# Optimization experiments

Hardware: AMD Instinct MI355X
Metric: run time of the kernel (lower is better)

The kernel has to match this reference:

```python
import jax, jax.numpy as jnp
import numpy as np

N_NODES = 50000   # gates in the circuit batch
N_HOPS = 100000   # number of k-hop cones
MAX_PI = 8        # max PIs per hop (padded, masked via stats == -1)
D = 128           # token_emb / hidden
D_FF = 4 * D      # cls_head hidden width (512)
TT = 64           # max_tt_len -> logits width
LN_EPS = 1e-5


def setup_inputs() -> dict:
    key = jax.random.key(0)
    ks = jax.random.split(key, 8)
    hf = jax.random.normal(ks[0], (N_NODES, D), jnp.float32)
    all_hop_pi = jax.random.randint(ks[1], (N_HOPS, MAX_PI), 0, N_NODES)
    # stats in {-1, 0, 1}; -1 marks an invalid (padded) PI slot
    all_hop_pi_stats = jax.random.randint(ks[2], (N_HOPS, MAX_PI), 0, 3) - 1
    all_hop_po = jax.random.randint(ks[3], (N_HOPS,), 0, N_NODES)
    w_q = jax.random.normal(ks[4], (D,), jnp.float32) / np.sqrt(D)
    W1 = jax.random.normal(ks[5], (D, D_FF), jnp.float32) / np.sqrt(D)
    b1 = jnp.zeros((D_FF,), jnp.float32)
    gamma = jnp.ones((D_FF,), jnp.float32)
    beta = jnp.zeros((D_FF,), jnp.float32)
    W2 = jax.random.normal(ks[6], (D_FF, TT), jnp.float32) / np.sqrt(D_FF)
    b2 = jnp.zeros((TT,), jnp.float32)
    return {
        'hf': hf, 'w_q': w_q, 'W1': W1, 'b1': b1, 'gamma': gamma,
        'beta': beta, 'W2': W2, 'b2': b2,
        'all_hop_pi': all_hop_pi, 'all_hop_pi_stats': all_hop_pi_stats,
        'all_hop_po': all_hop_po,
    }


def reference(hf, w_q, W1, b1, gamma, beta, W2, b2,
              all_hop_pi, all_hop_pi_stats, all_hop_po):
    # Per-hop gather: valid PI embeddings + PO embedding -> [H, P+1, D]
    pi_tok = hf[all_hop_pi]                       # [H, P, D]
    po_tok = hf[all_hop_po][:, None, :]           # [H, 1, D]
    tokens = jnp.concatenate([pi_tok, po_tok], axis=1)
    valid = jnp.concatenate(
        [all_hop_pi_stats != -1,
         jnp.ones((all_hop_po.shape[0], 1), bool)], axis=1)  # [H, P+1]
    # tf_Pooling: masked single-query attention pooling over the ragged set
    scores = jnp.einsum('hpd,d->hp', tokens, w_q) / jnp.sqrt(jnp.float32(D))
    scores = jnp.where(valid, scores, jnp.float32(-1e30))
    attn = jax.nn.softmax(scores, axis=-1)
    hop_hf = jnp.einsum('hp,hpd->hd', attn, tokens)  # [H, D]
    # cls_head: Linear(D, 4D) -> ReLU -> LayerNorm(4D) -> Linear(4D, TT)
    h = jax.nn.relu(hop_hf @ W1 + b1)
    mu = jnp.mean(h, axis=-1, keepdims=True)
    var = jnp.var(h, axis=-1, keepdims=True)
    h = (h - mu) * jax.lax.rsqrt(var + LN_EPS) * gamma + beta
    logits = h @ W2 + b2                           # [H, TT]
    return logits
```

## Files before the change

### kernel.cpp

```cpp
#include <hip/hip_runtime.h>
#include <hip/hip_bf16.h>
#include <math.h>

#define DIM 128
#define DFF 512
#define TTW 64
#define NPI 8
#define NTOK 9
#define TILE_H 32

typedef __attribute__((ext_vector_type(8))) short short8;
typedef __attribute__((ext_vector_type(4))) float float4v;

__device__ __forceinline__ float bf16lo_f32(unsigned u) {
    union { unsigned u; float f; } v; v.u = u << 16;
    return v.f;
}
__device__ __forceinline__ float bf16hi_f32(unsigned u) {
    union { unsigned u; float f; } v; v.u = u & 0xffff0000u;
    return v.f;
}
__device__ __forceinline__ unsigned pk_bf16(float a, float b) {
    __hip_bfloat162 h = __float22bfloat162_rn(float2{a, b});
    union { __hip_bfloat162 h; unsigned u; } cv; cv.h = h;
    return cv.u;
}

__global__ __launch_bounds__(256)
void prep_k(const float* __restrict__ hf, const float* __restrict__ W1,
            const float* __restrict__ W2,
            unsigned short* __restrict__ hf2, unsigned short* __restrict__ w1t,
            unsigned short* __restrict__ w2t,
            int n_hf, int B_HF)
{
    __shared__ float tile[32][33];
    const int b = blockIdx.x, t = threadIdx.x;
    if (b < B_HF) {
        int i = (b * 256 + t) * 8;
        if (i < n_hf) {
            float4v v0 = *(const float4v*)(hf + i);
            float4v v1 = *(const float4v*)(hf + i + 4);
            uint4 o;
            o.x = pk_bf16(v0[0], v0[1]);
            o.y = pk_bf16(v0[2], v0[3]);
            o.z = pk_bf16(v1[0], v1[1]);
            o.w = pk_bf16(v1[2], v1[3]);
            *(uint4*)(hf2 + i) = o;
        }
    } else if (b < B_HF + 64) {
        const int tb = b - B_HF;
        const int r0 = (tb & 3) * 32, c0 = (tb >> 2) * 32;
        const int ty = t >> 3, tx = t & 7;
        *(float4v*)&tile[ty][tx * 4] = *(const float4v*)(W1 + (r0 + ty) * DFF + c0 + tx * 4);
        __syncthreads();
        uint2 o;
        o.x = pk_bf16(tile[tx * 4 + 0][ty], tile[tx * 4 + 1][ty]);
        o.y = pk_bf16(tile[tx * 4 + 2][ty], tile[tx * 4 + 3][ty]);
        *(uint2*)(w1t + (c0 + ty) * DIM + r0 + tx * 4) = o;
    } else {
        const int tb = b - B_HF - 64;
        const int r0 = (tb & 15) * 32, c0 = (tb >> 4) * 32;
        const int ty = t >> 3, tx = t & 7;
        *(float4v*)&tile[ty][tx * 4] = *(const float4v*)(W2 + (r0 + ty) * TTW + c0 + tx * 4);
        __syncthreads();
        uint2 o;
        o.x = pk_bf16(tile[tx * 4 + 0][ty], tile[tx * 4 + 1][ty]);
        o.y = pk_bf16(tile[tx * 4 + 2][ty], tile[tx * 4 + 3][ty]);
        *(uint2*)(w2t + (c0 + ty) * DFF + r0 + tx * 4) = o;
    }
}

__global__ __launch_bounds__(256, 3)
void fused_k(const unsigned short* __restrict__ hf2,
             const float* __restrict__ w_q,
             const int* __restrict__ pi,
             const int* __restrict__ stats,
             const int* __restrict__ po,
             const unsigned short* __restrict__ w1t,
             const float* __restrict__ b1,
             const float* __restrict__ gamma,
             const float* __restrict__ beta,
             const unsigned short* __restrict__ w2t,
             const float* __restrict__ b2,
             float* __restrict__ out,
             int H)
{
    __shared__ __align__(16) unsigned short Apool[TILE_H][DIM + 8];
    __shared__ __align__(16) unsigned short Hsm[TILE_H][DFF + 8];
    __shared__ float part[2][16][4][2];

    const int t    = threadIdx.x;
    const int lane = t & 63;
    const int w    = t >> 6;
    const int row  = lane & 15;
    const int quad = lane >> 4;
    const int hop0 = blockIdx.x * TILE_H;

    {
        const int g = t >> 5, l = t & 31;
        const float4v wq4 = *(const float4v*)(w_q + l * 4);

        int idxs[4][NTOK];
        unsigned vm[4];
        #pragma unroll
        for (int it = 0; it < 4; ++it) {
            int hop = hop0 + g + it * 8;
            if (hop >= H) hop = H - 1;
            int4 p0 = *(const int4*)(pi + hop * NPI);
            int4 p1 = *(const int4*)(pi + hop * NPI + 4);
            int4 s0 = *(const int4*)(stats + hop * NPI);
            int4 s1 = *(const int4*)(stats + hop * NPI + 4);
            idxs[it][0] = p0.x; idxs[it][1] = p0.y;
            idxs[it][2] = p0.z; idxs[it][3] = p0.w;
            idxs[it][4] = p1.x; idxs[it][5] = p1.y;
            idxs[it][6] = p1.z; idxs[it][7] = p1.w;
            idxs[it][8] = po[hop];
            vm[it] = (s0.x != -1 ? 1u   : 0u) | (s0.y != -1 ? 2u   : 0u)
                   | (s0.z != -1 ? 4u   : 0u) | (s0.w != -1 ? 8u   : 0u)
                   | (s1.x != -1 ? 16u  : 0u) | (s1.y != -1 ? 32u  : 0u)
                   | (s1.z != -1 ? 64u  : 0u) | (s1.w != -1 ? 128u : 0u)
                   | 256u;
        }
        uint2 tu[4][NTOK];
        #pragma unroll
        for (int it = 0; it < 4; ++it)
            #pragma unroll
            for (int p = 0; p < NTOK; ++p)
                tu[it][p] = *(const uint2*)(hf2 + (size_t)idxs[it][p] * DIM + l * 4);

        #pragma unroll
        for (int it = 0; it < 4; ++it) {
            const int hl = g + it * 8;
            float tok[NTOK][4];
            #pragma unroll
            for (int p = 0; p < NTOK; ++p) {
                tok[p][0] = bf16lo_f32(tu[it][p].x);
                tok[p][1] = bf16hi_f32(tu[it][p].x);
                tok[p][2] = bf16lo_f32(tu[it][p].y);
                tok[p][3] = bf16hi_f32(tu[it][p].y);
            }
            float sc[NTOK];
            #pragma unroll
            for (int p = 0; p < NTOK; ++p)
                sc[p] = tok[p][0]*wq4[0] + tok[p][1]*wq4[1]
                      + tok[p][2]*wq4[2] + tok[p][3]*wq4[3];
            #pragma unroll
            for (int m = 1; m < 32; m <<= 1) {
                #pragma unroll
                for (int p = 0; p < NTOK; ++p) sc[p] += __shfl_xor(sc[p], m);
            }
            const float isd = 0.08838834764831845f;
            float mx = -1e30f;
            #pragma unroll
            for (int p = 0; p < NTOK; ++p) {
                sc[p] = ((vm[it] >> p) & 1u) ? sc[p] * isd : -1e30f;
                mx = fmaxf(mx, sc[p]);
            }
            float se = 0.f;
            #pragma unroll
            for (int p = 0; p < NTOK; ++p) { sc[p] = __expf(sc[p] - mx); se += sc[p]; }
            const float inv = 1.f / se;
            float a0=0.f, a1=0.f, a2=0.f, a3=0.f;
            #pragma unroll
            for (int p = 0; p < NTOK; ++p) {
                float a = sc[p] * inv;
                a0 += a * tok[p][0]; a1 += a * tok[p][1];
                a2 += a * tok[p][2]; a3 += a * tok[p][3];
            }
            uint2 o;
            o.x = pk_bf16(a0, a1);
            o.y = pk_bf16(a2, a3);
            *(uint2*)&Apool[hl][l * 4] = o;
        }
    }
    __syncthreads();

    float4v acc[8][2];
    #pragma unroll
    for (int mt = 0; mt < 8; ++mt) {
        acc[mt][0] = (float4v){0.f, 0.f, 0.f, 0.f};
        acc[mt][1] = (float4v){0.f, 0.f, 0.f, 0.f};
    }
    {
        short8 bfr[2][4];
        #pragma unroll
        for (int ks = 0; ks < 4; ++ks) {
            const int k0 = ks * 32 + quad * 8;
            #pragma unroll
            for (int ht = 0; ht < 2; ++ht)
                bfr[ht][ks] = *(const short8*)&Apool[ht * 16 + row][k0];
        }
        #pragma unroll
        for (int mt = 0; mt < 8; ++mt) {
            const unsigned short* wrow = w1t + (size_t)(w * 128 + mt * 16 + row) * DIM;
            #pragma unroll
            for (int ks = 0; ks < 4; ++ks) {
                short8 afr = *(const short8*)(wrow + ks * 32 + quad * 8);
                acc[mt][0] = __builtin_amdgcn_mfma_f32_16x16x32_bf16(afr, bfr[0][ks], acc[mt][0], 0, 0, 0);
                acc[mt][1] = __builtin_amdgcn_mfma_f32_16x16x32_bf16(afr, bfr[1][ks], acc[mt][1], 0, 0, 0);
            }
        }
    }
    float sum0 = 0.f, ssq0 = 0.f, sum1 = 0.f, ssq1 = 0.f;
    #pragma unroll
    for (int mt = 0; mt < 8; ++mt) {
        const int nb = w * 128 + mt * 16 + quad * 4;
        const float4v bias = *(const float4v*)(b1 + nb);
        #pragma unroll
        for (int r = 0; r < 4; ++r) {
            float v0 = fmaxf(acc[mt][0][r] + bias[r], 0.f);
            float v1 = fmaxf(acc[mt][1][r] + bias[r], 0.f);
            acc[mt][0][r] = v0;  sum0 += v0;  ssq0 += v0 * v0;
            acc[mt][1][r] = v1;  sum1 += v1;  ssq1 += v1 * v1;
        }
    }
    #pragma unroll
    for (int m = 16; m <= 32; m <<= 1) {
        sum0 += __shfl_xor(sum0, m);  ssq0 += __shfl_xor(ssq0, m);
        sum1 += __shfl_xor(sum1, m);  ssq1 += __shfl_xor(ssq1, m);
    }
    if (lane < 16) {
        part[0][row][w][0] = sum0;  part[0][row][w][1] = ssq0;
        part[1][row][w][0] = sum1;  part[1][row][w][1] = ssq1;
    }
    __syncthreads();
    float mu[2], rs[2];
    #pragma unroll
    for (int ht = 0; ht < 2; ++ht) {
        float S = 0.f, Q = 0.f;
        #pragma unroll
        for (int ww = 0; ww < 4; ++ww) {
            S += part[ht][row][ww][0];
            Q += part[ht][row][ww][1];
        }
        const float invn = 1.f / (float)DFF;
        mu[ht] = S * invn;
        float var = Q * invn - mu[ht] * mu[ht];
        rs[ht] = rsqrtf(var + 1e-5f);
    }
    #pragma unroll
    for (int mt = 0; mt < 8; ++mt) {
        const int nb = w * 128 + mt * 16 + quad * 4;
        const float4v g4  = *(const float4v*)(gamma + nb);
        const float4v be4 = *(const float4v*)(beta + nb);
        #pragma unroll
        for (int ht = 0; ht < 2; ++ht) {
            float o[4];
            #pragma unroll
            for (int r = 0; r < 4; ++r) {
                float tg = rs[ht] * g4[r];
                o[r] = acc[mt][ht][r] * tg + (be4[r] - mu[ht] * tg);
            }
            uint2 p;
            p.x = pk_bf16(o[0], o[1]);
            p.y = pk_bf16(o[2], o[3]);
            *(uint2*)&Hsm[ht * 16 + row][nb] = p;
        }
    }
    __syncthreads();

    {
        float4v acc2[2];
        acc2[0] = (float4v){0.f,0.f,0.f,0.f};
        acc2[1] = (float4v){0.f,0.f,0.f,0.f};
        #pragma unroll
        for (int ks = 0; ks < 16; ++ks) {
            const int k0 = ks * 32 + quad * 8;
            short8 bfr = *(const short8*)(w2t + (size_t)(w * 16 + row) * DFF + k0);
            #pragma unroll
            for (int mt = 0; mt < 2; ++mt) {
                short8 afr = *(const short8*)&Hsm[mt * 16 + row][k0];
                acc2[mt] = __builtin_amdgcn_mfma_f32_16x16x32_bf16(
                    afr, bfr, acc2[mt], 0, 0, 0);
            }
        }
        const float bb = b2[w * 16 + row];
        #pragma unroll
        for (int mt = 0; mt < 2; ++mt) {
            #pragma unroll
            for (int r = 0; r < 4; ++r) {
                int hop = hop0 + mt * 16 + quad * 4 + r;
                if (hop < H)
                    out[(size_t)hop * TTW + w * 16 + row] = acc2[mt][r] + bb;
            }
        }
    }
}

extern "C" void kernel_launch(void* const* d_in, const int* in_sizes, int n_in,
                              void* d_out, int out_size, void* d_ws, size_t ws_size,
                              hipStream_t stream) {
    const float* hf    = (const float*)d_in[0];
    const float* w_q   = (const float*)d_in[1];
    const float* W1    = (const float*)d_in[2];
    const float* b1    = (const float*)d_in[3];
    const float* gamma = (const float*)d_in[4];
    const float* beta  = (const float*)d_in[5];
    const float* W2    = (const float*)d_in[6];
    const float* b2    = (const float*)d_in[7];
    const int* pi      = (const int*)d_in[8];
    const int* stats   = (const int*)d_in[9];
    const int* po      = (const int*)d_in[10];
    float* out         = (float*)d_out;

    const int n_hf = in_sizes[0];
    const int H    = in_sizes[10];
    const int ntiles = (H + TILE_H - 1) / TILE_H;

    char* ws = (char*)d_ws;
    unsigned short* w1t = (unsigned short*)ws;
    unsigned short* w2t = (unsigned short*)(ws + 131072);
    unsigned short* hf2 = (unsigned short*)(ws + 196608);

    const int B_HF = (n_hf + 2047) / 2048;
    hipLaunchKernelGGL(prep_k, dim3(B_HF + 96), dim3(256), 0, stream,
                       hf, W1, W2, hf2, w1t, w2t, n_hf, B_HF);
    hipLaunchKernelGGL(fused_k, dim3(ntiles), dim3(256), 0, stream,
                       hf2, w_q, pi, stats, po, w1t, b1, gamma, beta, w2t, b2, out, H);
}
```

Measured before the change: 207.3 us.

## Merge prep and fused kernels into one cooperative persistent kernel with grid sync

Replaces the separate prep kernel launch with a cooperative launch in which every block first converts its share of hf, W1 and W2 to bf16, then waits at a grid-wide barrier. After the barrier, blocks loop persistently over hop tiles. The goal is to remove the second kernel launch and the gap between launches. In exchange it adds per-call host queries for occupancy and device attributes, a grid-sync cost, and a persistent loop with fewer blocks in flight. The old two-kernel path remains as a fallback.

Result: slower. 736.2 us (+255.2%).

```diff
diff --git a/kernel.cpp b/kernel.cpp
--- a/kernel.cpp
+++ b/kernel.cpp
@@ -1,6 +1,9 @@
 #include <hip/hip_runtime.h>
 #include <hip/hip_bf16.h>
+#include <hip/hip_cooperative_groups.h>
 #include <math.h>
+
+namespace cg = cooperative_groups;
 
 #define DIM 128
 #define DFF 512
@@ -70,220 +73,267 @@
     }
 }
 
+template<bool COOP>
 __global__ __launch_bounds__(256, 3)
-void fused_k(const unsigned short* __restrict__ hf2,
+void fused_t(const float* __restrict__ hf,
              const float* __restrict__ w_q,
              const int* __restrict__ pi,
              const int* __restrict__ stats,
              const int* __restrict__ po,
-             const unsigned short* __restrict__ w1t,
+             const float* __restrict__ W1,
+             const float* __restrict__ W2,
              const float* __restrict__ b1,
              const float* __restrict__ gamma,
              const float* __restrict__ beta,
-             const unsigned short* __restrict__ w2t,
              const float* __restrict__ b2,
+             unsigned short* __restrict__ hf2,
+             unsigned short* __restrict__ w1t,
+             unsigned short* __restrict__ w2t,
              float* __restrict__ out,
-             int H)
+             int H, int ntiles, int n_hf)
 {
     __shared__ __align__(16) unsigned short Apool[TILE_H][DIM + 8];
     __shared__ __align__(16) unsigned short Hsm[TILE_H][DFF + 8];
     __shared__ float part[2][16][4][2];
+    float (*tile)[33] = (float (*)[33])&Apool[0][0];
 
     const int t    = threadIdx.x;
     const int lane = t & 63;
     const int w    = t >> 6;
     const int row  = lane & 15;
     const int quad = lane >> 4;
-    const int hop0 = blockIdx.x * TILE_H;
-
-    {
-        const int g = t >> 5, l = t & 31;
-        const float4v wq4 = *(const float4v*)(w_q + l * 4);
-
-        int idxs[4][NTOK];
-        unsigned vm[4];
-        #pragma unroll
-        for (int it = 0; it < 4; ++it) {
-            int hop = hop0 + g + it * 8;
-            if (hop >= H) hop = H - 1;
-            int4 p0 = *(const int4*)(pi + hop * NPI);
-            int4 p1 = *(const int4*)(pi + hop * NPI + 4);
-            int4 s0 = *(const int4*)(stats + hop * NPI);
-            int4 s1 = *(const int4*)(stats + hop * NPI + 4);
-            idxs[it][0] = p0.x; idxs[it][1] = p0.y;
-            idxs[it][2] = p0.z; idxs[it][3] = p0.w;
-            idxs[it][4] = p1.x; idxs[it][5] = p1.y;
-            idxs[it][6] = p1.z; idxs[it][7] = p1.w;
-            idxs[it][8] = po[hop];
-            vm[it] = (s0.x != -1 ? 1u   : 0u) | (s0.y != -1 ? 2u   : 0u)
-                   | (s0.z != -1 ? 4u   : 0u) | (s0.w != -1 ? 8u   : 0u)
-                   | (s1.x != -1 ? 16u  : 0u) | (s1.y != -1 ? 32u  : 0u)
-                   | (s1.z != -1 ? 64u  : 0u) | (s1.w != -1 ? 128u : 0u)
-                   | 256u;
-        }
-        uint2 tu[4][NTOK];
-        #pragma unroll
-        for (int it = 0; it < 4; ++it)
-            #pragma unroll
-            for (int p = 0; p < NTOK; ++p)
-                tu[it][p] = *(const uint2*)(hf2 + (size_t)idxs[it][p] * DIM + l * 4);
-
-        #pragma unroll
-        for (int it = 0; it < 4; ++it) {
-            const int hl = g + it * 8;
-            float tok[NTOK][4];
-            #pragma unroll
-            for (int p = 0; p < NTOK; ++p) {
-                tok[p][0] = bf16lo_f32(tu[it][p].x);
-                tok[p][1] = bf16hi_f32(tu[it][p].x);
-                tok[p][2] = bf16lo_f32(tu[it][p].y);
-                tok[p][3] = bf16hi_f32(tu[it][p].y);
-            }
-            float sc[NTOK];
-            #pragma unroll
-            for (int p = 0; p < NTOK; ++p)
-                sc[p] = tok[p][0]*wq4[0] + tok[p][1]*wq4[1]
-                      + tok[p][2]*wq4[2] + tok[p][3]*wq4[3];
-            #pragma unroll
-            for (int m = 1; m < 32; m <<= 1) {
-                #pragma unroll
-                for (int p = 0; p < NTOK; ++p) sc[p] += __shfl_xor(sc[p], m);
-            }
-            const float isd = 0.08838834764831845f;
-            float mx = -1e30f;
-            #pragma unroll
-            for (int p = 0; p < NTOK; ++p) {
-                sc[p] = ((vm[it] >> p) & 1u) ? sc[p] * isd : -1e30f;
-                mx = fmaxf(mx, sc[p]);
-            }
-            float se = 0.f;
-            #pragma unroll
-            for (int p = 0; p < NTOK; ++p) { sc[p] = __expf(sc[p] - mx); se += sc[p]; }
-            const float inv = 1.f / se;
-            float a0=0.f, a1=0.f, a2=0.f, a3=0.f;
-            #pragma unroll
-            for (int p = 0; p < NTOK; ++p) {
-                float a = sc[p] * inv;
-                a0 += a * tok[p][0]; a1 += a * tok[p][1];
-                a2 += a * tok[p][2]; a3 += a * tok[p][3];
-            }
+
+    if constexpr (COOP) {
+        const int stride = gridDim.x * 256 * 8;
+        for (int i = (blockIdx.x * 256 + t) * 8; i < n_hf; i += stride) {
+            float4v v0 = *(const float4v*)(hf + i);
+            float4v v1 = *(const float4v*)(hf + i + 4);
+            uint4 o;
+            o.x = pk_bf16(v0[0], v0[1]);
+            o.y = pk_bf16(v0[2], v0[3]);
+            o.z = pk_bf16(v1[0], v1[1]);
+            o.w = pk_bf16(v1[2], v1[3]);
+            *(uint4*)(hf2 + i) = o;
+        }
+        if (blockIdx.x < 64) {
+            const int tb = blockIdx.x;
+            const int r0 = (tb & 3) * 32, c0 = (tb >> 2) * 32;
+            const int ty = t >> 3, tx = t & 7;
+            *(float4v*)&tile[ty][tx * 4] = *(const float4v*)(W1 + (r0 + ty) * DFF + c0 + tx * 4);
+            __syncthreads();
             uint2 o;
-            o.x = pk_bf16(a0, a1);
-            o.y = pk_bf16(a2, a3);
-            *(uint2*)&Apool[hl][l * 4] = o;
-        }
+            o.x = pk_bf16(tile[tx * 4 + 0][ty], tile[tx * 4 + 1][ty]);
+            o.y = pk_bf16(tile[tx * 4 + 2][ty], tile[tx * 4 + 3][ty]);
+            *(uint2*)(w1t + (c0 + ty) * DIM + r0 + tx * 4) = o;
+        } else if (blockIdx.x < 96) {
+            const int tb = blockIdx.x - 64;
+            const int r0 = (tb & 15) * 32, c0 = (tb >> 4) * 32;
+            const int ty = t >> 3, tx = t & 7;
+            *(float4v*)&tile[ty][tx * 4] = *(const float4v*)(W2 + (r0 + ty) * TTW + c0 + tx * 4);
+            __syncthreads();
+            uint2 o;
+            o.x = pk_bf16(tile[tx * 4 + 0][ty], tile[tx * 4 + 1][ty]);
+            o.y = pk_bf16(tile[tx * 4 + 2][ty], tile[tx * 4 + 3][ty]);
+            *(uint2*)(w2t + (c0 + ty) * DFF + r0 + tx * 4) = o;
+        }
+        __threadfence();
+        cg::this_grid().sync();
+        __syncthreads();
     }
-    __syncthreads();
-
-    float4v acc[8][2];
-    #pragma unroll
-    for (int mt = 0; mt < 8; ++mt) {
-        acc[mt][0] = (float4v){0.f, 0.f, 0.f, 0.f};
-        acc[mt][1] = (float4v){0.f, 0.f, 0.f, 0.f};
-    }
-    {
-        short8 bfr[2][4];
-        #pragma unroll
-        for (int ks = 0; ks < 4; ++ks) {
-            const int k0 = ks * 32 + quad * 8;
-            #pragma unroll
-            for (int ht = 0; ht < 2; ++ht)
-                bfr[ht][ks] = *(const short8*)&Apool[ht * 16 + row][k0];
-        }
+
+    for (int tilei = blockIdx.x; tilei < ntiles; tilei += (COOP ? gridDim.x : ntiles + 1)) {
+        const int hop0 = tilei * TILE_H;
+
+        {
+            const int g = t >> 5, l = t & 31;
+            const float4v wq4 = *(const float4v*)(w_q + l * 4);
+
+            int idxs[4][NTOK];
+            unsigned vm[4];
+            #pragma unroll
+            for (int it = 0; it < 4; ++it) {
+                int hop = hop0 + g + it * 8;
+                if (hop >= H) hop = H - 1;
+                int4 p0 = *(const int4*)(pi + hop * NPI);
+                int4 p1 = *(const int4*)(pi + hop * NPI + 4);
+                int4 s0 = *(const int4*)(stats + hop * NPI);
+                int4 s1 = *(const int4*)(stats + hop * NPI + 4);
+                idxs[it][0] = p0.x; idxs[it][1] = p0.y;
+                idxs[it][2] = p0.z; idxs[it][3] = p0.w;
+                idxs[it][4] = p1.x; idxs[it][5] = p1.y;
+                idxs[it][6] = p1.z; idxs[it][7] = p1.w;
+                idxs[it][8] = po[hop];
+                vm[it] = (s0.x != -1 ? 1u   : 0u) | (s0.y != -1 ? 2u   : 0u)
+                       | (s0.z != -1 ? 4u   : 0u) | (s0.w != -1 ? 8u   : 0u)
+                       | (s1.x != -1 ? 16u  : 0u) | (s1.y != -1 ? 32u  : 0u)
+                       | (s1.z != -1 ? 64u  : 0u) | (s1.w != -1 ? 128u : 0u)
+                       | 256u;
+            }
+            uint2 tu[4][NTOK];
+            #pragma unroll
+            for (int it = 0; it < 4; ++it)
+                #pragma unroll
+                for (int p = 0; p < NTOK; ++p)
+                    tu[it][p] = *(const uint2*)(hf2 + (size_t)idxs[it][p] * DIM + l * 4);
+
+            #pragma unroll
+            for (int it = 0; it < 4; ++it) {
+                const int hl = g + it * 8;
+                float tok[NTOK][4];
+                #pragma unroll
+                for (int p = 0; p < NTOK; ++p) {
+                    tok[p][0] = bf16lo_f32(tu[it][p].x);
+                    tok[p][1] = bf16hi_f32(tu[it][p].x);
+                    tok[p][2] = bf16lo_f32(tu[it][p].y);
+                    tok[p][3] = bf16hi_f32(tu[it][p].y);
+                }
+                float sc[NTOK];
+                #pragma unroll
+                for (int p = 0; p < NTOK; ++p)
+                    sc[p] = tok[p][0]*wq4[0] + tok[p][1]*wq4[1]
+                          + tok[p][2]*wq4[2] + tok[p][3]*wq4[3];
+                #pragma unroll
+                for (int m = 1; m < 32; m <<= 1) {
+                    #pragma unroll
+                    for (int p = 0; p < NTOK; ++p) sc[p] += __shfl_xor(sc[p], m);
+                }
+                const float isd = 0.08838834764831845f;
+                float mx = -1e30f;
+                #pragma unroll
+                for (int p = 0; p < NTOK; ++p) {
+                    sc[p] = ((vm[it] >> p) & 1u) ? sc[p] * isd : -1e30f;
+                    mx = fmaxf(mx, sc[p]);
+                }
+                float se = 0.f;
+                #pragma unroll
+                for (int p = 0; p < NTOK; ++p) { sc[p] = __expf(sc[p] - mx); se += sc[p]; }
+                const float inv = 1.f / se;
+                float a0=0.f, a1=0.f, a2=0.f, a3=0.f;
+                #pragma unroll
+                for (int p = 0; p < NTOK; ++p) {
+                    float a = sc[p] * inv;
+                    a0 += a * tok[p][0]; a1 += a * tok[p][1];
+                    a2 += a * tok[p][2]; a3 += a * tok[p][3];
+                }
+                uint2 o;
+                o.x = pk_bf16(a0, a1);
+                o.y = pk_bf16(a2, a3);
+                *(uint2*)&Apool[hl][l * 4] = o;
+            }
+        }
+        __syncthreads();
+
+        float4v acc[8][2];
         #pragma unroll
         for (int mt = 0; mt < 8; ++mt) {
-            const unsigned short* wrow = w1t + (size_t)(w * 128 + mt * 16 + row) * DIM;
+            acc[mt][0] = (float4v){0.f, 0.f, 0.f, 0.f};
+            acc[mt][1] = (float4v){0.f, 0.f, 0.f, 0.f};
+        }
+        {
+            short8 bfr[2][4];
             #pragma unroll
             for (int ks = 0; ks < 4; ++ks) {
-                short8 afr = *(const short8*)(wrow + ks * 32 + quad * 8);
-                acc[mt][0] = __builtin_amdgcn_mfma_f32_16x16x32_bf16(afr, bfr[0][ks], acc[mt][0], 0, 0, 0);
-                acc[mt][1] = __builtin_amdgcn_mfma_f32_16x16x32_bf16(afr, bfr[1][ks], acc[mt][1], 0, 0, 0);
-            }
-        }
-    }
-    float sum0 = 0.f, ssq0 = 0.f, sum1 = 0.f, ssq1 = 0.f;
-    #pragma unroll
-    for (int mt = 0; mt < 8; ++mt) {
-        const int nb = w * 128 + mt * 16 + quad * 4;
-        const float4v bias = *(const float4v*)(b1 + nb);
-        #pragma unroll
-        for (int r = 0; r < 4; ++r) {
-            float v0 = fmaxf(acc[mt][0][r] + bias[r], 0.f);
-            float v1 = fmaxf(acc[mt][1][r] + bias[r], 0.f);
-            acc[mt][0][r] = v0;  sum0 += v0;  ssq0 += v0 * v0;
-            acc[mt][1][r] = v1;  sum1 += v1;  ssq1 += v1 * v1;
-        }
-    }
-    #pragma unroll
-    for (int m = 16; m <= 32; m <<= 1) {
-        sum0 += __shfl_xor(sum0, m);  ssq0 += __shfl_xor(ssq0, m);
-        sum1 += __shfl_xor(sum1, m);  ssq1 += __shfl_xor(ssq1, m);
-    }
-    if (lane < 16) {
-        part[0][row][w][0] = sum0;  part[0][row][w][1] = ssq0;
-        part[1][row][w][0] = sum1;  part[1][row][w][1] = ssq1;
-    }
-    __syncthreads();
-    float mu[2], rs[2];
-    #pragma unroll
-    for (int ht = 0; ht < 2; ++ht) {
-        float S = 0.f, Q = 0.f;
-        #pragma unroll
-        for (int ww = 0; ww < 4; ++ww) {
-            S += part[ht][row][ww][0];
-            Q += part[ht][row][ww][1];
-        }
-        const float invn = 1.f / (float)DFF;
-        mu[ht] = S * invn;
-        float var = Q * invn - mu[ht] * mu[ht];
-        rs[ht] = rsqrtf(var + 1e-5f);
-    }
-    #pragma unroll
-    for (int mt = 0; mt < 8; ++mt) {
-        const int nb = w * 128 + mt * 16 + quad * 4;
-        const float4v g4  = *(const float4v*)(gamma + nb);
-        const float4v be4 = *(const float4v*)(beta + nb);
+                const int k0 = ks * 32 + quad * 8;
+                #pragma unroll
+                for (int ht = 0; ht < 2; ++ht)
+                    bfr[ht][ks] = *(const short8*)&Apool[ht * 16 + row][k0];
+            }
+            #pragma unroll
+            for (int mt = 0; mt < 8; ++mt) {
+                const unsigned short* wrow = w1t + (size_t)(w * 128 + mt * 16 + row) * DIM;
+                #pragma unroll
+                for (int ks = 0; ks < 4; ++ks) {
+                    short8 afr = *(const short8*)(wrow + ks * 32 + quad * 8);
+                    acc[mt][0] = __builtin_amdgcn_mfma_f32_16x16x32_bf16(afr, bfr[0][ks], acc[mt][0], 0, 0, 0);
+                    acc[mt][1] = __builtin_amdgcn_mfma_f32_16x16x32_bf16(afr, bfr[1][ks], acc[mt][1], 0, 0, 0);
+                }
+            }
+        }
+        float sum0 = 0.f, ssq0 = 0.f, sum1 = 0.f, ssq1 = 0.f;
+        #pragma unroll
+        for (int mt = 0; mt < 8; ++mt) {
+            const int nb = w * 128 + mt * 16 + quad * 4;
+            const float4v bias = *(const float4v*)(b1 + nb);
+            #pragma unroll
+            for (int r = 0; r < 4; ++r) {
+                float v0 = fmaxf(acc[mt][0][r] + bias[r], 0.f);
+                float v1 = fmaxf(acc[mt][1][r] + bias[r], 0.f);
+                acc[mt][0][r] = v0;  sum0 += v0;  ssq0 += v0 * v0;
+                acc[mt][1][r] = v1;  sum1 += v1;  ssq1 += v1 * v1;
+            }
+        }
+        #pragma unroll
+        for (int m = 16; m <= 32; m <<= 1) {
+            sum0 += __shfl_xor(sum0, m);  ssq0 += __shfl_xor(ssq0, m);
+            sum1 += __shfl_xor(sum1, m);  ssq1 += __shfl_xor(ssq1, m);
+        }
+        if (lane < 16) {
+            part[0][row][w][0] = sum0;  part[0][row][w][1] = ssq0;
+            part[1][row][w][0] = sum1;  part[1][row][w][1] = ssq1;
+        }
+        __syncthreads();
+        float mu[2], rs[2];
         #pragma unroll
         for (int ht = 0; ht < 2; ++ht) {
-            float o[4];
-            #pragma unroll
-            for (int r = 0; r < 4; ++r) {
-                float tg = rs[ht] * g4[r];
-                o[r] = acc[mt][ht][r] * tg + (be4[r] - mu[ht] * tg);
-            }
-            uint2 p;
-            p.x = pk_bf16(o[0], o[1]);
-            p.y = pk_bf16(o[2], o[3]);
-            *(uint2*)&Hsm[ht * 16 + row][nb] = p;
-        }
-    }
-    __syncthreads();
-
-    {
-        float4v acc2[2];
-        acc2[0] = (float4v){0.f,0.f,0.f,0.f};
-        acc2[1] = (float4v){0.f,0.f,0.f,0.f};
-        #pragma unroll
-        for (int ks = 0; ks < 16; ++ks) {
-            const int k0 = ks * 32 + quad * 8;
-            short8 bfr = *(const short8*)(w2t + (size_t)(w * 16 + row) * DFF + k0);
+            float S = 0.f, Q = 0.f;
+            #pragma unroll
+            for (int ww = 0; ww < 4; ++ww) {
+                S += part[ht][row][ww][0];
+                Q += part[ht][row][ww][1];
+            }
+            const float invn = 1.f / (float)DFF;
+            mu[ht] = S * invn;
+            float var = Q * invn - mu[ht] * mu[ht];
+            rs[ht] = rsqrtf(var + 1e-5f);
+        }
+        #pragma unroll
+        for (int mt = 0; mt < 8; ++mt) {
+            const int nb = w * 128 + mt * 16 + quad * 4;
+            const float4v g4  = *(const float4v*)(gamma + nb);
+            const float4v be4 = *(const float4v*)(beta + nb);
+            #pragma unroll
+            for (int ht = 0; ht < 2; ++ht) {
+                float o[4];
+                #pragma unroll
+                for (int r = 0; r < 4; ++r) {
+                    float tg = rs[ht] * g4[r];
+                    o[r] = acc[mt][ht][r] * tg + (be4[r] - mu[ht] * tg);
+                }
+                uint2 p;
+                p.x = pk_bf16(o[0], o[1]);
+                p.y = pk_bf16(o[2], o[3]);
+                *(uint2*)&Hsm[ht * 16 + row][nb] = p;
+            }
+        }
+        __syncthreads();
+
+        {
+            float4v acc2[2];
+            acc2[0] = (float4v){0.f,0.f,0.f,0.f};
+            acc2[1] = (float4v){0.f,0.f,0.f,0.f};
+            #pragma unroll
+            for (int ks = 0; ks < 16; ++ks) {
+                const int k0 = ks * 32 + quad * 8;
+                short8 bfr = *(const short8*)(w2t + (size_t)(w * 16 + row) * DFF + k0);
+                #pragma unroll
+                for (int mt = 0; mt < 2; ++mt) {
+                    short8 afr = *(const short8*)&Hsm[mt * 16 + row][k0];
+                    acc2[mt] = __builtin_amdgcn_mfma_f32_16x16x32_bf16(
+                        afr, bfr, acc2[mt], 0, 0, 0);
+                }
+            }
+            const float bb = b2[w * 16 + row];
             #pragma unroll
             for (int mt = 0; mt < 2; ++mt) {
-                short8 afr = *(const short8*)&Hsm[mt * 16 + row][k0];
-                acc2[mt] = __builtin_amdgcn_mfma_f32_16x16x32_bf16(
-                    afr, bfr, acc2[mt], 0, 0, 0);
-            }
-        }
-        const float bb = b2[w * 16 + row];
-        #pragma unroll
-        for (int mt = 0; mt < 2; ++mt) {
-            #pragma unroll
-            for (int r = 0; r < 4; ++r) {
-                int hop = hop0 + mt * 16 + quad * 4 + r;
-                if (hop < H)
-                    out[(size_t)hop * TTW + w * 16 + row] = acc2[mt][r] + bb;
-            }
-        }
+                #pragma unroll
+                for (int r = 0; r < 4; ++r) {
+                    int hop = hop0 + mt * 16 + quad * 4 + r;
+                    if (hop < H)
+                        out[(size_t)hop * TTW + w * 16 + row] = acc2[mt][r] + bb;
+                }
+            }
+        }
+        if (COOP) __syncthreads();
     }
 }
 
@@ -303,18 +353,44 @@
     const int* po      = (const int*)d_in[10];
     float* out         = (float*)d_out;
 
-    const int n_hf = in_sizes[0];
-    const int H    = in_sizes[10];
-    const int ntiles = (H + TILE_H - 1) / TILE_H;
+    int n_hf = in_sizes[0];
+    int H    = in_sizes[10];
+    int ntiles = (H + TILE_H - 1) / TILE_H;
 
     char* ws = (char*)d_ws;
     unsigned short* w1t = (unsigned short*)ws;
     unsigned short* w2t = (unsigned short*)(ws + 131072);
     unsigned short* hf2 = (unsigned short*)(ws + 196608);
 
+    int coop_attr = 0, dev = 0;
+    hipGetDevice(&dev);
+    hipDeviceGetAttribute(&coop_attr, hipDeviceAttributeCooperativeLaunch, dev);
+    int maxb = 0;
+    hipError_t oe = hipOccupancyMaxActiveBlocksPerMultiprocessor(
+        &maxb, fused_t<true>, 256, 0);
+
+    if (coop_attr && oe == hipSuccess && maxb >= 2) {
+        const int maxgrid = 256 * maxb;
+        int tpb  = (ntiles + maxgrid - 1) / maxgrid;
+        int grid = (ntiles + tpb - 1) / tpb;
+        if (grid >= 97) {
+            void* args[] = {
+                (void*)&hf, (void*)&w_q, (void*)&pi, (void*)&stats, (void*)&po,
+                (void*)&W1, (void*)&W2, (void*)&b1, (void*)&gamma, (void*)&beta,
+                (void*)&b2, (void*)&hf2, (void*)&w1t, (void*)&w2t, (void*)&out,
+                (void*)&H, (void*)&ntiles, (void*)&n_hf
+            };
+            hipError_t le = hipLaunchCooperativeKernel((const void*)&fused_t<true>,
+                                                       dim3(grid), dim3(256),
+                                                       args, 0, stream);
+            if (le == hipSuccess) return;
+        }
+    }
+
     const int B_HF = (n_hf + 2047) / 2048;
     hipLaunchKernelGGL(prep_k, dim3(B_HF + 96), dim3(256), 0, stream,
                        hf, W1, W2, hf2, w1t, w2t, n_hf, B_HF);
-    hipLaunchKernelGGL(fused_k, dim3(ntiles), dim3(256), 0, stream,
-                       hf2, w_q, pi, stats, po, w1t, b1, gamma, beta, w2t, b2, out, H);
-}
+    hipLaunchKernelGGL((fused_t<false>), dim3(ntiles), dim3(256), 0, stream,
+                       hf, w_q, pi, stats, po, W1, W2, b1, gamma, beta, b2,
+                       hf2, w1t, w2t, out, H, ntiles, n_hf);
+}
```

## Double fused kernel block to 512 threads, splitting per-warp work in half

Applied to the files above, without the earlier changes.

The fused gather-pool-MLP kernel moves from 256 to 512 threads per block while keeping 32 hops per tile. Each wave now gathers two hops instead of four, computes 64 instead of 128 FFN columns in the first GEMM, and owns a single 16x16 output tile in the second GEMM. LayerNorm partial sums are reduced across 8 waves instead of 4. The aim is more parallelism and more loads in flight per block with fewer registers per thread. The cost is more waves each doing less work, and each B2 fragment is now loaded by two waves.

After: 237.5 us. +14.6%, slower.

```diff
diff --git a/kernel.cpp b/kernel.cpp
--- a/kernel.cpp
+++ b/kernel.cpp
@@ -8,6 +8,7 @@
 #define NPI 8
 #define NTOK 9
 #define TILE_H 32
+#define THREADS 512
 
 typedef __attribute__((ext_vector_type(8))) short short8;
 typedef __attribute__((ext_vector_type(4))) float float4v;
@@ -70,7 +71,7 @@
     }
 }
 
-__global__ __launch_bounds__(256, 3)
+__global__ __launch_bounds__(THREADS, 4)
 void fused_k(const unsigned short* __restrict__ hf2,
              const float* __restrict__ w_q,
              const int* __restrict__ pi,
@@ -87,7 +88,7 @@
 {
     __shared__ __align__(16) unsigned short Apool[TILE_H][DIM + 8];
     __shared__ __align__(16) unsigned short Hsm[TILE_H][DFF + 8];
-    __shared__ float part[2][16][4][2];
+    __shared__ float part[2][16][8][2];
 
     const int t    = threadIdx.x;
     const int lane = t & 63;
@@ -100,11 +101,11 @@
         const int g = t >> 5, l = t & 31;
         const float4v wq4 = *(const float4v*)(w_q + l * 4);
 
-        int idxs[4][NTOK];
-        unsigned vm[4];
-        #pragma unroll
-        for (int it = 0; it < 4; ++it) {
-            int hop = hop0 + g + it * 8;
+        int idxs[2][NTOK];
+        unsigned vm[2];
+        #pragma unroll
+        for (int it = 0; it < 2; ++it) {
+            int hop = hop0 + g + it * 16;
             if (hop >= H) hop = H - 1;
             int4 p0 = *(const int4*)(pi + hop * NPI);
             int4 p1 = *(const int4*)(pi + hop * NPI + 4);
@@ -121,16 +122,16 @@
                    | (s1.z != -1 ? 64u  : 0u) | (s1.w != -1 ? 128u : 0u)
                    | 256u;
         }
-        uint2 tu[4][NTOK];
-        #pragma unroll
-        for (int it = 0; it < 4; ++it)
+        uint2 tu[2][NTOK];
+        #pragma unroll
+        for (int it = 0; it < 2; ++it)
             #pragma unroll
             for (int p = 0; p < NTOK; ++p)
                 tu[it][p] = *(const uint2*)(hf2 + (size_t)idxs[it][p] * DIM + l * 4);
 
         #pragma unroll
-        for (int it = 0; it < 4; ++it) {
-            const int hl = g + it * 8;
+        for (int it = 0; it < 2; ++it) {
+            const int hl = g + it * 16;
             float tok[NTOK][4];
             #pragma unroll
             for (int p = 0; p < NTOK; ++p) {
@@ -175,9 +176,9 @@
     }
     __syncthreads();
 
-    float4v acc[8][2];
-    #pragma unroll
-    for (int mt = 0; mt < 8; ++mt) {
+    float4v acc[4][2];
+    #pragma unroll
+    for (int mt = 0; mt < 4; ++mt) {
         acc[mt][0] = (float4v){0.f, 0.f, 0.f, 0.f};
         acc[mt][1] = (float4v){0.f, 0.f, 0.f, 0.f};
     }
@@ -191,8 +192,8 @@
                 bfr[ht][ks] = *(const short8*)&Apool[ht * 16 + row][k0];
         }
         #pragma unroll
-        for (int mt = 0; mt < 8; ++mt) {
-            const unsigned short* wrow = w1t + (size_t)(w * 128 + mt * 16 + row) * DIM;
+        for (int mt = 0; mt < 4; ++mt) {
+            const unsigned short* wrow = w1t + (size_t)(w * 64 + mt * 16 + row) * DIM;
             #pragma unroll
             for (int ks = 0; ks < 4; ++ks) {
                 short8 afr = *(const short8*)(wrow + ks * 32 + quad * 8);
@@ -203,8 +204,8 @@
     }
     float sum0 = 0.f, ssq0 = 0.f, sum1 = 0.f, ssq1 = 0.f;
     #pragma unroll
-    for (int mt = 0; mt < 8; ++mt) {
-        const int nb = w * 128 + mt * 16 + quad * 4;
+    for (int mt = 0; mt < 4; ++mt) {
+        const int nb = w * 64 + mt * 16 + quad * 4;
         const float4v bias = *(const float4v*)(b1 + nb);
         #pragma unroll
         for (int r = 0; r < 4; ++r) {
@@ -229,7 +230,7 @@
     for (int ht = 0; ht < 2; ++ht) {
         float S = 0.f, Q = 0.f;
         #pragma unroll
-        for (int ww = 0; ww < 4; ++ww) {
+        for (int ww = 0; ww < 8; ++ww) {
             S += part[ht][row][ww][0];
             Q += part[ht][row][ww][1];
         }
@@ -239,8 +240,8 @@
         rs[ht] = rsqrtf(var + 1e-5f);
     }
     #pragma unroll
-    for (int mt = 0; mt < 8; ++mt) {
-        const int nb = w * 128 + mt * 16 + quad * 4;
+    for (int mt = 0; mt < 4; ++mt) {
+        const int nb = w * 64 + mt * 16 + quad * 4;
         const float4v g4  = *(const float4v*)(gamma + nb);
         const float4v be4 = *(const float4v*)(beta + nb);
         #pragma unroll
@@ -260,29 +261,22 @@
     __syncthreads();
 
     {
-        float4v acc2[2];
-        acc2[0] = (float4v){0.f,0.f,0.f,0.f};
-        acc2[1] = (float4v){0.f,0.f,0.f,0.f};
+        const int mtile = w >> 2;
+        const int ttile = w & 3;
+        float4v acc2 = (float4v){0.f,0.f,0.f,0.f};
         #pragma unroll
         for (int ks = 0; ks < 16; ++ks) {
             const int k0 = ks * 32 + quad * 8;
-            short8 bfr = *(const short8*)(w2t + (size_t)(w * 16 + row) * DFF + k0);
-            #pragma unroll
-            for (int mt = 0; mt < 2; ++mt) {
-                short8 afr = *(const short8*)&Hsm[mt * 16 + row][k0];
-                acc2[mt] = __builtin_amdgcn_mfma_f32_16x16x32_bf16(
-                    afr, bfr, acc2[mt], 0, 0, 0);
-            }
-        }
-        const float bb = b2[w * 16 + row];
-        #pragma unroll
-        for (int mt = 0; mt < 2; ++mt) {
-            #pragma unroll
-            for (int r = 0; r < 4; ++r) {
-                int hop = hop0 + mt * 16 + quad * 4 + r;
-                if (hop < H)
-                    out[(size_t)hop * TTW + w * 16 + row] = acc2[mt][r] + bb;
-            }
+            short8 bfr = *(const short8*)(w2t + (size_t)(ttile * 16 + row) * DFF + k0);
+            short8 afr = *(const short8*)&Hsm[mtile * 16 + row][k0];
+            acc2 = __builtin_amdgcn_mfma_f32_16x16x32_bf16(afr, bfr, acc2, 0, 0, 0);
+        }
+        const float bb = b2[ttile * 16 + row];
+        #pragma unroll
+        for (int r = 0; r < 4; ++r) {
+            int hop = hop0 + mtile * 16 + quad * 4 + r;
+            if (hop < H)
+                out[(size_t)hop * TTW + ttile * 16 + row] = acc2[r] + bb;
         }
     }
 }
@@ -315,6 +309,6 @@
     const int B_HF = (n_hf + 2047) / 2048;
     hipLaunchKernelGGL(prep_k, dim3(B_HF + 96), dim3(256), 0, stream,
                        hf, W1, W2, hf2, w1t, w2t, n_hf, B_HF);
-    hipLaunchKernelGGL(fused_k, dim3(ntiles), dim3(256), 0, stream,
+    hipLaunchKernelGGL(fused_k, dim3(ntiles), dim3(THREADS), 0, stream,
                        hf2, w_q, pi, stats, po, w1t, b1, gamma, beta, w2t, b2, out, H);
 }
```

## Gather fp32 hf rows directly instead of pre-converting hf to bf16

Applied to the files above, without the earlier changes.

Removes the prep pass that converted the whole hf table (50000x128) to bf16, and has the fused kernel gather fp32 rows directly with float4 loads. This drops a full read plus a half-size write of hf and the dependency between the two launches. In exchange the gather traffic in the fused kernel doubles (16B per lane per token instead of 8B). The loads are also no longer batched across all four hops up front, which lowers register pressure but reduces memory-level parallelism.

Measured after the change: 231.6 us. +11.7%, slower.

```diff
diff --git a/kernel.cpp b/kernel.cpp
--- a/kernel.cpp
+++ b/kernel.cpp
@@ -12,14 +12,6 @@
 typedef __attribute__((ext_vector_type(8))) short short8;
 typedef __attribute__((ext_vector_type(4))) float float4v;
 
-__device__ __forceinline__ float bf16lo_f32(unsigned u) {
-    union { unsigned u; float f; } v; v.u = u << 16;
-    return v.f;
-}
-__device__ __forceinline__ float bf16hi_f32(unsigned u) {
-    union { unsigned u; float f; } v; v.u = u & 0xffff0000u;
-    return v.f;
-}
 __device__ __forceinline__ unsigned pk_bf16(float a, float b) {
     __hip_bfloat162 h = __float22bfloat162_rn(float2{a, b});
     union { __hip_bfloat162 h; unsigned u; } cv; cv.h = h;
@@ -27,28 +19,13 @@
 }
 
 __global__ __launch_bounds__(256)
-void prep_k(const float* __restrict__ hf, const float* __restrict__ W1,
-            const float* __restrict__ W2,
-            unsigned short* __restrict__ hf2, unsigned short* __restrict__ w1t,
-            unsigned short* __restrict__ w2t,
-            int n_hf, int B_HF)
+void prep_k(const float* __restrict__ W1, const float* __restrict__ W2,
+            unsigned short* __restrict__ w1t, unsigned short* __restrict__ w2t)
 {
     __shared__ float tile[32][33];
     const int b = blockIdx.x, t = threadIdx.x;
-    if (b < B_HF) {
-        int i = (b * 256 + t) * 8;
-        if (i < n_hf) {
-            float4v v0 = *(const float4v*)(hf + i);
-            float4v v1 = *(const float4v*)(hf + i + 4);
-            uint4 o;
-            o.x = pk_bf16(v0[0], v0[1]);
-            o.y = pk_bf16(v0[2], v0[3]);
-            o.z = pk_bf16(v1[0], v1[1]);
-            o.w = pk_bf16(v1[2], v1[3]);
-            *(uint4*)(hf2 + i) = o;
-        }
-    } else if (b < B_HF + 64) {
-        const int tb = b - B_HF;
+    if (b < 64) {
+        const int tb = b;
         const int r0 = (tb & 3) * 32, c0 = (tb >> 2) * 32;
         const int ty = t >> 3, tx = t & 7;
         *(float4v*)&tile[ty][tx * 4] = *(const float4v*)(W1 + (r0 + ty) * DFF + c0 + tx * 4);
@@ -58,7 +35,7 @@
         o.y = pk_bf16(tile[tx * 4 + 2][ty], tile[tx * 4 + 3][ty]);
         *(uint2*)(w1t + (c0 + ty) * DIM + r0 + tx * 4) = o;
     } else {
-        const int tb = b - B_HF - 64;
+        const int tb = b - 64;
         const int r0 = (tb & 15) * 32, c0 = (tb >> 4) * 32;
         const int ty = t >> 3, tx = t & 7;
         *(float4v*)&tile[ty][tx * 4] = *(const float4v*)(W2 + (r0 + ty) * TTW + c0 + tx * 4);
@@ -71,7 +48,7 @@
 }
 
 __global__ __launch_bounds__(256, 3)
-void fused_k(const unsigned short* __restrict__ hf2,
+void fused_k(const float* __restrict__ hf,
              const float* __restrict__ w_q,
              const int* __restrict__ pi,
              const int* __restrict__ stats,
@@ -99,46 +76,32 @@
     {
         const int g = t >> 5, l = t & 31;
         const float4v wq4 = *(const float4v*)(w_q + l * 4);
-
-        int idxs[4][NTOK];
-        unsigned vm[4];
         #pragma unroll
         for (int it = 0; it < 4; ++it) {
-            int hop = hop0 + g + it * 8;
+            const int hl = g + it * 8;
+            int hop = hop0 + hl;
             if (hop >= H) hop = H - 1;
-            int4 p0 = *(const int4*)(pi + hop * NPI);
-            int4 p1 = *(const int4*)(pi + hop * NPI + 4);
-            int4 s0 = *(const int4*)(stats + hop * NPI);
-            int4 s1 = *(const int4*)(stats + hop * NPI + 4);
-            idxs[it][0] = p0.x; idxs[it][1] = p0.y;
-            idxs[it][2] = p0.z; idxs[it][3] = p0.w;
-            idxs[it][4] = p1.x; idxs[it][5] = p1.y;
-            idxs[it][6] = p1.z; idxs[it][7] = p1.w;
-            idxs[it][8] = po[hop];
-            vm[it] = (s0.x != -1 ? 1u   : 0u) | (s0.y != -1 ? 2u   : 0u)
+            int idx[NTOK];
+            unsigned vm;
+            {
+                int4 p0 = *(const int4*)(pi + hop * NPI);
+                int4 p1 = *(const int4*)(pi + hop * NPI + 4);
+                int4 s0 = *(const int4*)(stats + hop * NPI);
+                int4 s1 = *(const int4*)(stats + hop * NPI + 4);
+                idx[0]=p0.x; idx[1]=p0.y; idx[2]=p0.z; idx[3]=p0.w;
+                idx[4]=p1.x; idx[5]=p1.y; idx[6]=p1.z; idx[7]=p1.w;
+                idx[8]=po[hop];
+                vm = (s0.x != -1 ? 1u   : 0u) | (s0.y != -1 ? 2u   : 0u)
                    | (s0.z != -1 ? 4u   : 0u) | (s0.w != -1 ? 8u   : 0u)
                    | (s1.x != -1 ? 16u  : 0u) | (s1.y != -1 ? 32u  : 0u)
                    | (s1.z != -1 ? 64u  : 0u) | (s1.w != -1 ? 128u : 0u)
                    | 256u;
-        }
-        uint2 tu[4][NTOK];
-        #pragma unroll
-        for (int it = 0; it < 4; ++it)
+            }
+            float4v tok[NTOK];
             #pragma unroll
             for (int p = 0; p < NTOK; ++p)
-                tu[it][p] = *(const uint2*)(hf2 + (size_t)idxs[it][p] * DIM + l * 4);
-
-        #pragma unroll
-        for (int it = 0; it < 4; ++it) {
-            const int hl = g + it * 8;
-            float tok[NTOK][4];
-            #pragma unroll
-            for (int p = 0; p < NTOK; ++p) {
-                tok[p][0] = bf16lo_f32(tu[it][p].x);
-                tok[p][1] = bf16hi_f32(tu[it][p].x);
-                tok[p][2] = bf16lo_f32(tu[it][p].y);
-                tok[p][3] = bf16hi_f32(tu[it][p].y);
-            }
+                tok[p] = *(const float4v*)(hf + (size_t)idx[p] * DIM + l * 4);
+
             float sc[NTOK];
             #pragma unroll
             for (int p = 0; p < NTOK; ++p)
@@ -153,7 +116,7 @@
             float mx = -1e30f;
             #pragma unroll
             for (int p = 0; p < NTOK; ++p) {
-                sc[p] = ((vm[it] >> p) & 1u) ? sc[p] * isd : -1e30f;
+                sc[p] = ((vm >> p) & 1u) ? sc[p] * isd : -1e30f;
                 mx = fmaxf(mx, sc[p]);
             }
             float se = 0.f;
@@ -303,18 +266,14 @@
     const int* po      = (const int*)d_in[10];
     float* out         = (float*)d_out;
 
-    const int n_hf = in_sizes[0];
-    const int H    = in_sizes[10];
+    const int H = in_sizes[10];
     const int ntiles = (H + TILE_H - 1) / TILE_H;
 
     char* ws = (char*)d_ws;
     unsigned short* w1t = (unsigned short*)ws;
     unsigned short* w2t = (unsigned short*)(ws + 131072);
-    unsigned short* hf2 = (unsigned short*)(ws + 196608);
-
-    const int B_HF = (n_hf + 2047) / 2048;
-    hipLaunchKernelGGL(prep_k, dim3(B_HF + 96), dim3(256), 0, stream,
-                       hf, W1, W2, hf2, w1t, w2t, n_hf, B_HF);
+
+    hipLaunchKernelGGL(prep_k, dim3(96), dim3(256), 0, stream, W1, W2, w1t, w2t);
     hipLaunchKernelGGL(fused_k, dim3(ntiles), dim3(256), 0, stream,
-                       hf2, w_q, pi, stats, po, w1t, b1, gamma, beta, w2t, b2, out, H);
-}
+                       hf, w_q, pi, stats, po, w1t, b1, gamma, beta, w2t, b2, out, H);
+}
```
